# Optimization experiments

Measured on AMD Instinct MI355X. Metric: run time of the kernel, lower is better.

## Reference

```python
import jax, jax.numpy as jnp
import numpy as np

# Dimensions (TinyLlama-like)
B, T = 4, 1024
D = 2048          # hidden_size
H, DH = 32, 64    # heads, head_dim
HK = 8            # kv heads (GQA, n_rep = 4)
RQ, RKV = 32, 32  # per-head SVD ranks
RO, RF = 1024, 1024
I = 5632          # intermediate_size
THETA = 10000.0
EPS = 1e-5


def setup_inputs() -> dict:
    key = jax.random.key(0)
    ks = jax.random.split(key, 16)
    p = lambda k, s: jax.random.normal(k, s, jnp.float32) * 0.02
    return {
        "x": jax.random.normal(ks[0], (B, T, D), jnp.float32),
        "ln1_w": jnp.ones((D,), jnp.float32),
        "ln2_w": jnp.ones((D,), jnp.float32),
        "q_Us": p(ks[1], (H, DH, RQ)),  "q_V": p(ks[2], (H, RQ, D)),
        "k_Us": p(ks[3], (HK, DH, RKV)), "k_V": p(ks[4], (HK, RKV, D)),
        "v_Us": p(ks[5], (HK, DH, RKV)), "v_V": p(ks[6], (HK, RKV, D)),
        "o_Us": p(ks[7], (D, RO)),  "o_V": p(ks[8], (RO, H * DH)),
        "g_Us": p(ks[9], (I, RF)),  "g_V": p(ks[10], (RF, D)),
        "u_Us": p(ks[11], (I, RF)), "u_V": p(ks[12], (RF, D)),
        "d_Us": p(ks[13], (D, RF)), "d_V": p(ks[14], (RF, I)),
    }


def _rms(x, w):
    return x * jax.lax.rsqrt(jnp.mean(x * x, axis=-1, keepdims=True) + EPS) * w


def _rope_cos_sin(t_len, dh, dtype):
    half = dh // 2
    inv_freq = 1.0 / (THETA ** (jnp.arange(half, dtype=jnp.float32) / half))
    ang = jnp.arange(t_len, dtype=jnp.float32)[:, None] * inv_freq[None, :]  # [T, half]
    return jnp.cos(ang).astype(dtype), jnp.sin(ang).astype(dtype)


def _apply_rope(x, cos, sin):
    # x: [B,h,T,Dh], LLaMA half-split rotation
    half = x.shape[-1] // 2
    x1, x2 = x[..., :half], x[..., half:]
    c = cos[None, None]  # [1,1,T,half]
    s = sin[None, None]
    return jnp.concatenate([x1 * c - x2 * s, x2 * c + x1 * s], axis=-1)


def reference(x, ln1_w, ln2_w, q_Us, q_V, k_Us, k_V, v_Us, v_V,
              o_Us, o_V, g_Us, g_V, u_Us, u_V, d_Us, d_V):
    b, t, d = x.shape
    h1 = _rms(x, ln1_w)

    # per-head low-rank projections: y_h = x @ V_h^T @ Us_h^T
    q = jnp.einsum('bhtr,hdr->bhtd', jnp.einsum('btD,hrD->bhtr', h1, q_V), q_Us)  # [B,H,T,Dh]
    k = jnp.einsum('bhtr,hdr->bhtd', jnp.einsum('btD,hrD->bhtr', h1, k_V), k_Us)  # [B,Hk,T,Dh]
    v = jnp.einsum('bhtr,hdr->bhtd', jnp.einsum('btD,hrD->bhtr', h1, v_V), v_Us)

    cos, sin = _rope_cos_sin(t, DH, x.dtype)
    q = _apply_rope(q, cos, sin)
    k = _apply_rope(k, cos, sin)

    n_rep = H // HK
    k = jnp.repeat(k, n_rep, axis=1)  # _repeat_kv
    v = jnp.repeat(v, n_rep, axis=1)

    scale = 1.0 / np.sqrt(DH)
    scores = jnp.einsum('bhtd,bhsd->bhts', q, k) * scale
    causal = jnp.tril(jnp.ones((t, t), bool))
    scores = jnp.where(causal[None, None], scores, jnp.finfo(scores.dtype).min)
    attn = jax.nn.softmax(scores, axis=-1)
    ctx = jnp.einsum('bhts,bhsd->bhtd', attn, v)
    ctx = ctx.transpose(0, 2, 1, 3).reshape(b, t, H * DH)

    # low-rank output proj: o = ctx @ o_V^T @ o_Us^T
    attn_out = jnp.einsum('btr,Dr->btD', jnp.einsum('btk,rk->btr', ctx, o_V), o_Us)
    x = x + attn_out

    # SwiGLU MLP with low-rank factors
    h2 = _rms(x, ln2_w)
    g = jnp.einsum('btr,ir->bti', jnp.einsum('btD,rD->btr', h2, g_V), g_Us)
    u = jnp.einsum('btr,ir->bti', jnp.einsum('btD,rD->btr', h2, u_V), u_Us)
    ff = jax.nn.silu(g) * u
    down = jnp.einsum('btr,Dr->btD', jnp.einsum('bti,ri->btr', ff, d_V), d_Us)
    return x + down
```

## Files before the change

kernel.cpp:

```cpp
#include <hip/hip_runtime.h>
#include <math.h>

typedef unsigned short u16;
typedef unsigned int u32;
typedef __bf16 bf16x8 __attribute__((ext_vector_type(8)));
typedef float f32x4 __attribute__((ext_vector_type(4)));

__device__ __forceinline__ float bf2f(u16 u) {
  union { u32 i; float f; } x; x.i = ((u32)u) << 16; return x.f;
}
__device__ __forceinline__ u16 f2bf(float f) {
  union { float f; u32 i; } x; x.f = f;
  return (u16)((x.i + 0x7fffu + ((x.i >> 16) & 1u)) >> 16);
}

#define GLDS16(gp, lp)                                                        \
  __builtin_amdgcn_global_load_lds(                                           \
      (const __attribute__((address_space(1))) u32*)(gp),                     \
      (__attribute__((address_space(3))) u32*)(lp), 16, 0, 0)

__global__ void detect_k(const u16* __restrict__ w, int* __restrict__ flag) {
  if (threadIdx.x == 0 && blockIdx.x == 0)
    *flag = (w[0] == 0x0000u && w[1] == 0x3F80u) ? 1 : 0;
}

struct CvtArgs {
  const void* src[17];
  u32 dstOff[17];
  u32 blkOff[18];
};

__global__ __launch_bounds__(256) void cvt_all(CvtArgs a, u16* __restrict__ dstB,
                                               const int* __restrict__ flag) {
  int seg = 0;
  const int bx = blockIdx.x;
#pragma unroll 1
  while (bx >= (int)a.blkOff[seg + 1]) seg++;
  const long local = ((long)(bx - a.blkOff[seg]) * 256 + threadIdx.x) * 8;
  u16* dst = dstB + a.dstOff[seg] + local;
  if (*flag) {
    const float* s = (const float*)a.src[seg] + local;
    float4 va = *(const float4*)(s);
    float4 vb = *(const float4*)(s + 4);
    uint4 o; u16* op = (u16*)&o;
    op[0] = f2bf(va.x); op[1] = f2bf(va.y); op[2] = f2bf(va.z); op[3] = f2bf(va.w);
    op[4] = f2bf(vb.x); op[5] = f2bf(vb.y); op[6] = f2bf(vb.z); op[7] = f2bf(vb.w);
    *(uint4*)dst = o;
  } else {
    *(uint4*)dst = *(const uint4*)((const u16*)a.src[seg] + local);
  }
}

__global__ __launch_bounds__(256) void rms_k(const u16* __restrict__ x,
                                             const u16* __restrict__ w,
                                             u16* __restrict__ out) {
  const long row = blockIdx.x;
  const u16* xr = x + row * 2048;
  u16* orow = out + row * 2048;
  const int tid = threadIdx.x;
  const int base = tid * 8;
  uint4 u = *(const uint4*)(xr + base);
  const u16* us = (const u16*)&u;
  float v[8];
  float ss = 0.f;
#pragma unroll
  for (int i = 0; i < 8; i++) { v[i] = bf2f(us[i]); ss += v[i] * v[i]; }
#pragma unroll
  for (int off = 32; off > 0; off >>= 1) ss += __shfl_xor(ss, off);
  __shared__ float red[4];
  if ((tid & 63) == 0) red[tid >> 6] = ss;
  __syncthreads();
  float total = red[0] + red[1] + red[2] + red[3];
  float inv = rsqrtf(total * (1.0f / 2048.0f) + 1e-5f);
  uint4 wv = *(const uint4*)(w + base);
  const u16* wp = (const u16*)&wv;
  uint4 o;
  u16* op = (u16*)&o;
#pragma unroll
  for (int i = 0; i < 8; i++) op[i] = f2bf(v[i] * inv * bf2f(wp[i]));
  *(uint4*)(orow + base) = o;
}

template <int EPI>
__global__ __launch_bounds__(256, 2) void gemm_bt(const u16* __restrict__ A,
                                                  const u16* __restrict__ B,
                                                  void* Cv,
                                                  const u16* R,
                                                  const int* flagp,
                                                  int N, int Klen, int lda, int ldb) {
  __shared__ u16 As[128 * 32];
  __shared__ u16 Bs[128 * 32];
  const int m0 = blockIdx.y * 128;
  const int n0 = blockIdx.x * 128;
  const int tid = threadIdx.x;
  const int wave = tid >> 6;
  const int lane = tid & 63;
  const int wr = (wave >> 1) * 64;
  const int wc = (wave & 1) * 64;
  const int l16 = lane & 15;
  const int quad = lane >> 4;
  u16* C = (u16*)Cv;
  float* Cf = (float*)Cv;
  bool f32o = false;
  if (EPI == 3) f32o = (*flagp != 0);

  f32x4 acc[4][4];
#pragma unroll
  for (int i = 0; i < 4; i++)
#pragma unroll
    for (int j = 0; j < 4; j++) acc[i][j] = (f32x4){0.f, 0.f, 0.f, 0.f};

  const int srow = wave * 16 + (lane >> 2);
  const int scol = (lane & 3) * 8;
  const u16* Ag = A + (long)(m0 + srow) * lda + scol;
  const u16* Bg = B + (long)(n0 + srow) * ldb + scol;
  const long astep = (long)64 * lda;
  const long bstep = (long)64 * ldb;
  u16* Asw = &As[wave * 16 * 32];
  u16* Bsw = &Bs[wave * 16 * 32];

  for (int k0 = 0; k0 < Klen; k0 += 32) {
    GLDS16(Ag + k0, Asw);
    GLDS16(Ag + astep + k0, Asw + 64 * 32);
    GLDS16(Bg + k0, Bsw);
    GLDS16(Bg + bstep + k0, Bsw + 64 * 32);
    __syncthreads();
    bf16x8 af[4], bfr[4];
#pragma unroll
    for (int t = 0; t < 4; t++) {
      af[t]  = *(const bf16x8*)(&As[(wr + t * 16 + l16) * 32 + quad * 8]);
      bfr[t] = *(const bf16x8*)(&Bs[(wc + t * 16 + l16) * 32 + quad * 8]);
    }
#pragma unroll
    for (int i = 0; i < 4; i++)
#pragma unroll
      for (int j = 0; j < 4; j++)
        acc[i][j] = __builtin_amdgcn_mfma_f32_16x16x32_bf16(bfr[j], af[i], acc[i][j], 0, 0, 0);
    __syncthreads();
  }

#pragma unroll
  for (int i = 0; i < 4; i++) {
    const int m = m0 + wr + i * 16 + l16;
#pragma unroll
    for (int j = 0; j < 4; j++) {
      const int n = n0 + wc + j * 16 + quad * 4;
      const long idx = (long)m * N + n;
      float v[4];
#pragma unroll
      for (int r = 0; r < 4; r++) v[r] = acc[i][j][r];
      if (EPI == 1 || EPI == 3) {
        uint2 rr = *(const uint2*)(R + idx);
        const u16* rp = (const u16*)&rr;
#pragma unroll
        for (int r = 0; r < 4; r++) v[r] += bf2f(rp[r]);
      }
      if (EPI == 3 && f32o) {
        float4 o = {v[0], v[1], v[2], v[3]};
        *(float4*)(Cf + idx) = o;
      } else {
        uint2 o; u16* op = (u16*)&o;
#pragma unroll
        for (int r = 0; r < 4; r++) op[r] = f2bf(v[r]);
        *(uint2*)(C + idx) = o;
      }
    }
  }
}

#define STAGE_SILU(buf, k0)                                                   \
  do {                                                                        \
    GLDS16(Ag_ + (k0), &Asg[buf][woff]);                                      \
    GLDS16(Ag_ + astep + (k0), &Asg[buf][woff + 64 * 32]);                    \
    GLDS16(Au_ + (k0), &Asu[buf][woff]);                                      \
    GLDS16(Au_ + astep + (k0), &Asu[buf][woff + 64 * 32]);                    \
    GLDS16(Bg_ + (k0), &Bsg[buf][woff]);                                      \
    GLDS16(Bg_ + bstep + (k0), &Bsg[buf][woff + 64 * 32]);                    \
    GLDS16(Bu_ + (k0), &Bsu[buf][woff]);                                      \
    GLDS16(Bu_ + bstep + (k0), &Bsu[buf][woff + 64 * 32]);                    \
  } while (0)

__global__ __launch_bounds__(256, 2) void gemm_silu(const u16* __restrict__ Agp,
                                                    const u16* __restrict__ Aup,
                                                    const u16* __restrict__ Bgp,
                                                    const u16* __restrict__ Bup,
                                                    u16* __restrict__ C,
                                                    int N, int Klen, int lda, int ldb) {
  __shared__ u16 Asg[2][128 * 32];
  __shared__ u16 Asu[2][128 * 32];
  __shared__ u16 Bsg[2][128 * 32];
  __shared__ u16 Bsu[2][128 * 32];
  const int m0 = blockIdx.y * 128;
  const int n0 = blockIdx.x * 128;
  const int tid = threadIdx.x;
  const int wave = tid >> 6;
  const int lane = tid & 63;
  const int wr = (wave >> 1) * 64;
  const int wc = (wave & 1) * 64;
  const int l16 = lane & 15;
  const int quad = lane >> 4;

  f32x4 ag[4][4], au[4][4];
#pragma unroll
  for (int i = 0; i < 4; i++)
#pragma unroll
    for (int j = 0; j < 4; j++) {
      ag[i][j] = (f32x4){0.f, 0.f, 0.f, 0.f};
      au[i][j] = (f32x4){0.f, 0.f, 0.f, 0.f};
    }

  const int srow = wave * 16 + (lane >> 2);
  const int scol = ((lane & 3) ^ ((lane >> 3) & 3)) * 8;
  const u16* Ag_ = Agp + (long)(m0 + srow) * lda + scol;
  const u16* Au_ = Aup + (long)(m0 + srow) * lda + scol;
  const u16* Bg_ = Bgp + (long)(n0 + srow) * ldb + scol;
  const u16* Bu_ = Bup + (long)(n0 + srow) * ldb + scol;
  const long astep = (long)64 * lda;
  const long bstep = (long)64 * ldb;
  const int woff = wave * 16 * 32;
  const int rsw = (quad ^ ((l16 >> 1) & 3)) * 8;

  const int nk = Klen >> 5;
  STAGE_SILU(0, 0);
  int cur = 0;
  for (int kt = 0; kt < nk; ++kt) {
    if (kt + 1 < nk) {
      STAGE_SILU(cur ^ 1, (kt + 1) << 5);
      asm volatile("s_waitcnt vmcnt(8)" ::: "memory");
    } else {
      asm volatile("s_waitcnt vmcnt(0)" ::: "memory");
    }
    asm volatile("s_barrier" ::: "memory");
    bf16x8 afg[4], afu[4], bfg[4], bfu[4];
#pragma unroll
    for (int t = 0; t < 4; t++) {
      afg[t] = *(const bf16x8*)(&Asg[cur][(wr + t * 16 + l16) * 32 + rsw]);
      afu[t] = *(const bf16x8*)(&Asu[cur][(wr + t * 16 + l16) * 32 + rsw]);
      bfg[t] = *(const bf16x8*)(&Bsg[cur][(wc + t * 16 + l16) * 32 + rsw]);
      bfu[t] = *(const bf16x8*)(&Bsu[cur][(wc + t * 16 + l16) * 32 + rsw]);
    }
#pragma unroll
    for (int i = 0; i < 4; i++)
#pragma unroll
      for (int j = 0; j < 4; j++) {
        ag[i][j] = __builtin_amdgcn_mfma_f32_16x16x32_bf16(bfg[j], afg[i], ag[i][j], 0, 0, 0);
        au[i][j] = __builtin_amdgcn_mfma_f32_16x16x32_bf16(bfu[j], afu[i], au[i][j], 0, 0, 0);
      }
    asm volatile("s_barrier" ::: "memory");
    cur ^= 1;
  }

#pragma unroll
  for (int i = 0; i < 4; i++) {
    const int m = m0 + wr + i * 16 + l16;
#pragma unroll
    for (int j = 0; j < 4; j++) {
      const int n = n0 + wc + j * 16 + quad * 4;
      const long idx = (long)m * N + n;
      uint2 o; u16* op = (u16*)&o;
#pragma unroll
      for (int r = 0; r < 4; r++) {
        float g = ag[i][j][r];
        float v = au[i][j][r] * g / (1.f + __expf(-g));
        op[r] = f2bf(v);
      }
      *(uint2*)(C + idx) = o;
    }
  }
}

__global__ __launch_bounds__(256) void combine2(const u16* __restrict__ a,
                                                const u16* __restrict__ b,
                                                u16* __restrict__ o) {
  const long i = ((long)blockIdx.x * 256 + threadIdx.x) * 8;
  uint4 ua = *(const uint4*)(a + i);
  uint4 ub = *(const uint4*)(b + i);
  const u16* pa = (const u16*)&ua;
  const u16* pb = (const u16*)&ub;
  uint4 uo; u16* po = (u16*)&uo;
#pragma unroll
  for (int j = 0; j < 8; j++) po[j] = f2bf(bf2f(pa[j]) + bf2f(pb[j]));
  *(uint4*)(o + i) = uo;
}

__global__ __launch_bounds__(256) void expand_k(const u16* __restrict__ rbuf,
                                                int rstride,
                                                const u16* __restrict__ Us,
                                                u16* __restrict__ out,
                                                int nheads, int doRope) {
  const int tok = blockIdx.x;
  const int wave = threadIdx.x >> 6;
  const int d = threadIdx.x & 63;
  const int h = blockIdx.y * 4 + wave;
  const int b = tok >> 10;
  const int t = tok & 1023;
  const u16* up = Us + ((long)h * 64 + d) * 32;
  const u16* rp = rbuf + (long)tok * rstride + h * 32;
  float s = 0.f;
#pragma unroll
  for (int c = 0; c < 4; c++) {
    uint4 uu = *(const uint4*)(up + c * 8);
    uint4 rr = *(const uint4*)(rp + c * 8);
    const u16* u8p = (const u16*)&uu;
    const u16* r8p = (const u16*)&rr;
#pragma unroll
    for (int i = 0; i < 8; i++) s += bf2f(u8p[i]) * bf2f(r8p[i]);
  }
  if (doRope) {
    const int j = d & 31;
    float inv = powf(10000.0f, -(float)j * (1.0f / 32.0f));
    float ang = (float)t * inv;
    float sn, cs;
    sincosf(ang, &sn, &cs);
    float partner = __shfl_xor(s, 32);
    s = (d < 32) ? (s * cs - partner * sn) : (s * cs + partner * sn);
  }
  out[(((long)(b * nheads + h)) * 1024 + t) * 64 + d] = f2bf(s);
}

__global__ __launch_bounds__(256) void vT_k(const u16* __restrict__ vbuf,
                                            u16* __restrict__ vT) {
  __shared__ u16 tile[64][72];
  const int b = blockIdx.z, kh = blockIdx.y;
  const int t0 = blockIdx.x * 64;
  const int tid = threadIdx.x;
  const int r = tid >> 2;
  const int c = (tid & 3) * 16;
  const u16* src = vbuf + ((long)(b * 8 + kh) * 1024 + t0 + r) * 64 + c;
  *(uint4*)&tile[r][c] = *(const uint4*)src;
  *(uint4*)&tile[r][c + 8] = *(const uint4*)(src + 8);
  __syncthreads();
  u16 tmp[16];
#pragma unroll
  for (int i = 0; i < 16; i++) tmp[i] = tile[c + i][r];
  u16* dst = vT + ((long)(b * 8 + kh) * 64 + r) * 1024 + t0 + c;
  *(uint4*)dst = *(uint4*)&tmp[0];
  *(uint4*)(dst + 8) = *(uint4*)&tmp[8];
}

#define ATS 72

__global__ __launch_bounds__(256, 2) void attn_mfma(const u16* __restrict__ q,
                                                    const u16* __restrict__ k,
                                                    const u16* __restrict__ vT,
                                                    u16* __restrict__ ctx) {
  __shared__ u16 Ks[64 * ATS];
  __shared__ u16 Vts[64 * ATS];
  __shared__ u16 Plds[4][16 * ATS];
  const int bx = blockIdx.x;
  const int h = blockIdx.y;
  const int b = blockIdx.z;
  const int kh = h >> 2;
  const int qlo = bx * 64;
  const int qhi = (15 - bx) * 64;
  const int tid = threadIdx.x;
  const int wave = tid >> 6;
  const int lane = tid & 63;
  const int l16 = lane & 15;
  const int quad = lane >> 4;

  const u16* qb = q + ((long)(b * 32 + h) * 1024) * 64;
  const u16* kb = k + ((long)(b * 8 + kh) * 1024) * 64;
  const u16* vb = vT + ((long)(b * 8 + kh) * 64) * 1024;

  bf16x8 qfl[2], qfh[2];
  {
    const u16* qp = qb + (long)(qlo + wave * 16 + l16) * 64 + quad * 8;
    qfl[0] = *(const bf16x8*)(qp);
    qfl[1] = *(const bf16x8*)(qp + 32);
    qp = qb + (long)(qhi + wave * 16 + l16) * 64 + quad * 8;
    qfh[0] = *(const bf16x8*)(qp);
    qfh[1] = *(const bf16x8*)(qp + 32);
  }

  float ml[4], ll[4], mh[4], lh[4];
  f32x4 ol[4], oh[4];
#pragma unroll
  for (int r = 0; r < 4; r++) { ml[r] = -1e30f; ll[r] = 0.f; mh[r] = -1e30f; lh[r] = 0.f; }
#pragma unroll
  for (int j = 0; j < 4; j++) { ol[j] = (f32x4){0.f, 0.f, 0.f, 0.f}; oh[j] = ol[j]; }

  const int srow = tid >> 2;
  const int sc0 = (tid & 3) * 16;
  int s0 = 0;

  auto process = [&](const bf16x8* qf, float* m, float* l, f32x4* oacc, int qtb) {
    f32x4 s[4];
#pragma unroll
    for (int t = 0; t < 4; t++) {
      s[t] = (f32x4){0.f, 0.f, 0.f, 0.f};
      const u16* kr = &Ks[(t * 16 + l16) * ATS + quad * 8];
      bf16x8 b0 = *(const bf16x8*)(kr);
      bf16x8 b1 = *(const bf16x8*)(kr + 32);
      s[t] = __builtin_amdgcn_mfma_f32_16x16x32_bf16(qf[0], b0, s[t], 0, 0, 0);
      s[t] = __builtin_amdgcn_mfma_f32_16x16x32_bf16(qf[1], b1, s[t], 0, 0, 0);
    }
#pragma unroll
    for (int t = 0; t < 4; t++) s[t] *= 0.125f;
    if (s0 == qtb) {
#pragma unroll
      for (int t = 0; t < 4; t++)
#pragma unroll
        for (int r = 0; r < 4; r++)
          if (s0 + t * 16 + l16 > qtb + wave * 16 + quad * 4 + r) s[t][r] = -1e30f;
    }
    float p[4][4];
#pragma unroll
    for (int r = 0; r < 4; r++) {
      float mx = fmaxf(fmaxf(s[0][r], s[1][r]), fmaxf(s[2][r], s[3][r]));
#pragma unroll
      for (int off = 1; off < 16; off <<= 1) mx = fmaxf(mx, __shfl_xor(mx, off));
      const float mnew = fmaxf(m[r], mx);
      const float alpha = __expf(m[r] - mnew);
      float ps = 0.f;
#pragma unroll
      for (int t = 0; t < 4; t++) { p[t][r] = __expf(s[t][r] - mnew); ps += p[t][r]; }
#pragma unroll
      for (int off = 1; off < 16; off <<= 1) ps += __shfl_xor(ps, off);
      l[r] = l[r] * alpha + ps;
      m[r] = mnew;
#pragma unroll
      for (int j = 0; j < 4; j++) oacc[j][r] *= alpha;
    }
    u16* pw = &Plds[wave][0];
#pragma unroll
    for (int t = 0; t < 4; t++)
#pragma unroll
      for (int r = 0; r < 4; r++)
        pw[(quad * 4 + r) * ATS + t * 16 + l16] = f2bf(p[t][r]);
    bf16x8 pf0 = *(const bf16x8*)(&pw[l16 * ATS + quad * 8]);
    bf16x8 pf1 = *(const bf16x8*)(&pw[l16 * ATS + 32 + quad * 8]);
#pragma unroll
    for (int j = 0; j < 4; j++) {
      const u16* vr = &Vts[(j * 16 + l16) * ATS + quad * 8];
      bf16x8 v0 = *(const bf16x8*)(vr);
      bf16x8 v1 = *(const bf16x8*)(vr + 32);
      oacc[j] = __builtin_amdgcn_mfma_f32_16x16x32_bf16(pf0, v0, oacc[j], 0, 0, 0);
      oacc[j] = __builtin_amdgcn_mfma_f32_16x16x32_bf16(pf1, v1, oacc[j], 0, 0, 0);
    }
  };

  for (s0 = 0; s0 <= qhi; s0 += 64) {
    __syncthreads();
    {
      const u16* kp = kb + (long)(s0 + srow) * 64 + sc0;
      *(uint4*)&Ks[srow * ATS + sc0] = *(const uint4*)kp;
      *(uint4*)&Ks[srow * ATS + sc0 + 8] = *(const uint4*)(kp + 8);
      const u16* vp = vb + (long)srow * 1024 + s0 + sc0;
      *(uint4*)&Vts[srow * ATS + sc0] = *(const uint4*)vp;
      *(uint4*)&Vts[srow * ATS + sc0 + 8] = *(const uint4*)(vp + 8);
    }
    __syncthreads();
    process(qfh, mh, lh, oh, qhi);
    if (s0 <= qlo) process(qfl, ml, ll, ol, qlo);
  }

#pragma unroll
  for (int r = 0; r < 4; r++) {
    const int rowl = qlo + wave * 16 + quad * 4 + r;
    const int rowh = qhi + wave * 16 + quad * 4 + r;
    const float il = 1.f / ll[r];
    const float ih = 1.f / lh[r];
#pragma unroll
    for (int j = 0; j < 4; j++) {
      ctx[(((long)(b * 1024 + rowl)) * 32 + h) * 64 + j * 16 + l16] = f2bf(ol[j][r] * il);
      ctx[(((long)(b * 1024 + rowh)) * 32 + h) * 64 + j * 16 + l16] = f2bf(oh[j][r] * ih);
    }
  }
}

extern "C" void kernel_launch(void* const* d_in, const int* in_sizes, int n_in,
                              void* d_out, int out_size, void* d_ws, size_t ws_size,
                              hipStream_t stream) {
  char* ws = (char*)d_ws;
  u16* cb = (u16*)ws;
  u16* cx    = cb + 0;
  u16* cln1  = cb + 8388608;
  u16* cln2  = cb + 8390656;
  u16* cqUs  = cb + 8392704;
  u16* ckUs  = cb + 8458240;
  u16* cvUs  = cb + 8474624;
  u16* cqkvV = cb + 8491008;
  u16* coUs  = cb + 11636736;
  u16* coV   = cb + 13733888;
  u16* cguV  = cb + 15831040;
  u16* cgUs  = cb + 20025344;
  u16* cuUs  = cb + 25792512;
  u16* cdUs  = cb + 31559680;
  u16* cdV   = cb + 33656832;

  char* P = ws + 78848000;
  u16* h1    = (u16*)(P + 0);
  u16* qkvr  = (u16*)(P + 16777216);
  u16* qp0   = (u16*)(P + 33554432);
  u16* qp1   = (u16*)(P + 46137344);
  u16* qbuf  = (u16*)(P + 33554432);
  u16* kbuf  = (u16*)(P + 50331648);
  u16* vbuf  = (u16*)(P + 54525952);
  u16* ctx   = (u16*)(P + 58720256);
  u16* vbufT = (u16*)(P + 75497472);
  u16* orr   = (u16*)(P + 75497472);
  u16* xmid  = (u16*)(P + 83886080);
  u16* op0   = (u16*)(P + 0);
  u16* op1   = (u16*)(P + 8388608);
  u16* h2    = (u16*)(P + 0);
  u16* gur   = (u16*)(P + 16777216);
  u16* gbuf  = (u16*)(P + 33554432);
  u16* dp0   = (u16*)(P + 0);
  u16* dp1   = (u16*)(P + 8388608);
  u16* dr    = (u16*)(P + 16777216);
  int* flag  = (int*)(ws + 179511296);

  const dim3 blk(256);
  detect_k<<<1, 64, 0, stream>>>((const u16*)d_in[1], flag);

  CvtArgs ca;
  const u32 dOff[17] = {0u, 8388608u, 8390656u, 8392704u, 8491008u, 8458240u,
                        10588160u, 8474624u, 11112448u, 11636736u, 13733888u,
                        20025344u, 15831040u, 25792512u, 17928192u, 31559680u,
                        33656832u};
  const u32 nblk[17] = {4096u, 1u, 1u, 32u, 1024u, 8u, 256u, 8u, 256u, 1024u,
                        1024u, 2816u, 1024u, 2816u, 1024u, 1024u, 2816u};
  u32 cum = 0;
  for (int i = 0; i < 17; i++) {
    ca.src[i] = d_in[i];
    ca.dstOff[i] = dOff[i];
    ca.blkOff[i] = cum;
    cum += nblk[i];
  }
  ca.blkOff[17] = cum;
  cvt_all<<<cum, blk, 0, stream>>>(ca, cb, flag);

  rms_k<<<4096, blk, 0, stream>>>(cx, cln1, h1);
  gemm_bt<0><<<dim3(12, 32), blk, 0, stream>>>(h1, cqkvV, qp0, nullptr, nullptr, 1536, 1024, 2048, 2048);
  gemm_bt<0><<<dim3(12, 32), blk, 0, stream>>>(h1 + 1024, cqkvV + 1024, qp1, nullptr, nullptr, 1536, 1024, 2048, 2048);
  combine2<<<3072, blk, 0, stream>>>(qp0, qp1, qkvr);
  expand_k<<<dim3(4096, 8), blk, 0, stream>>>(qkvr, 1536, cqUs, qbuf, 32, 1);
  expand_k<<<dim3(4096, 2), blk, 0, stream>>>(qkvr + 1024, 1536, ckUs, kbuf, 8, 1);
  expand_k<<<dim3(4096, 2), blk, 0, stream>>>(qkvr + 1280, 1536, cvUs, vbuf, 8, 0);
  vT_k<<<dim3(16, 8, 4), blk, 0, stream>>>(vbuf, vbufT);
  attn_mfma<<<dim3(8, 32, 4), blk, 0, stream>>>(qbuf, kbuf, vbufT, ctx);
  gemm_bt<0><<<dim3(8, 32), blk, 0, stream>>>(ctx, coV, op0, nullptr, nullptr, 1024, 1024, 2048, 2048);
  gemm_bt<0><<<dim3(8, 32), blk, 0, stream>>>(ctx + 1024, coV + 1024, op1, nullptr, nullptr, 1024, 1024, 2048, 2048);
  combine2<<<2048, blk, 0, stream>>>(op0, op1, orr);
  gemm_bt<1><<<dim3(16, 32), blk, 0, stream>>>(orr, coUs, xmid, cx, nullptr, 2048, 1024, 1024, 1024);
  rms_k<<<4096, blk, 0, stream>>>(xmid, cln2, h2);
  gemm_bt<0><<<dim3(16, 32), blk, 0, stream>>>(h2, cguV, gur, nullptr, nullptr, 2048, 2048, 2048, 2048);
  gemm_silu<<<dim3(44, 32), blk, 0, stream>>>(gur, gur + 1024, cgUs, cuUs, gbuf, 5632, 1024, 2048, 1024);
  gemm_bt<0><<<dim3(8, 32), blk, 0, stream>>>(gbuf, cdV, dp0, nullptr, nullptr, 1024, 2816, 5632, 5632);
  gemm_bt<0><<<dim3(8, 32), blk, 0, stream>>>(gbuf + 2816, cdV + 2816, dp1, nullptr, nullptr, 1024, 2816, 5632, 5632);
  combine2<<<2048, blk, 0, stream>>>(dp0, dp1, dr);
  gemm_bt<3><<<dim3(16, 32), blk, 0, stream>>>(dr, cdUs, d_out, xmid, flag, 2048, 1024, 1024, 1024);
}
```

Measured before the change: 854.5 us.

## Split gate and up GEMM across separate waves in fused SiLU kernel

The fused gate/up SiLU GEMM now uses 512 threads. Waves 0-3 compute the gate product and waves 4-7 compute the up product, each holding half the accumulators. The up results are passed to the gate waves through shared memory before the SiLU epilogue. This halves per-wave register pressure and doubles the waves per tile, aiming for better latency hiding. The cost is an extra shared-memory exchange and a block-wide sync at the end.

Result: no change. 851.8 us (-0.3%).

```diff
diff --git a/kernel.cpp b/kernel.cpp
--- a/kernel.cpp
+++ b/kernel.cpp
@@ -170,44 +170,38 @@
 
 #define STAGE_SILU(buf, k0)                                                   \
   do {                                                                        \
-    GLDS16(Ag_ + (k0), &Asg[buf][woff]);                                      \
-    GLDS16(Ag_ + astep + (k0), &Asg[buf][woff + 64 * 32]);                    \
-    GLDS16(Au_ + (k0), &Asu[buf][woff]);                                      \
-    GLDS16(Au_ + astep + (k0), &Asu[buf][woff + 64 * 32]);                    \
-    GLDS16(Bg_ + (k0), &Bsg[buf][woff]);                                      \
-    GLDS16(Bg_ + bstep + (k0), &Bsg[buf][woff + 64 * 32]);                    \
-    GLDS16(Bu_ + (k0), &Bsu[buf][woff]);                                      \
-    GLDS16(Bu_ + bstep + (k0), &Bsu[buf][woff + 64 * 32]);                    \
+    GLDS16(Ag_ + (k0), &SH[buf][0][woff]);                                    \
+    GLDS16(Au_ + (k0), &SH[buf][1][woff]);                                    \
+    GLDS16(Bg_ + (k0), &SH[buf][2][woff]);                                    \
+    GLDS16(Bu_ + (k0), &SH[buf][3][woff]);                                    \
   } while (0)
 
-__global__ __launch_bounds__(256, 2) void gemm_silu(const u16* __restrict__ Agp,
+__global__ __launch_bounds__(512, 4) void gemm_silu(const u16* __restrict__ Agp,
                                                     const u16* __restrict__ Aup,
                                                     const u16* __restrict__ Bgp,
                                                     const u16* __restrict__ Bup,
                                                     u16* __restrict__ C,
                                                     int N, int Klen, int lda, int ldb) {
-  __shared__ u16 Asg[2][128 * 32];
-  __shared__ u16 Asu[2][128 * 32];
-  __shared__ u16 Bsg[2][128 * 32];
-  __shared__ u16 Bsu[2][128 * 32];
+  __shared__ u16 SH[2][4][128 * 32];
   const int m0 = blockIdx.y * 128;
   const int n0 = blockIdx.x * 128;
   const int tid = threadIdx.x;
   const int wave = tid >> 6;
   const int lane = tid & 63;
-  const int wr = (wave >> 1) * 64;
-  const int wc = (wave & 1) * 64;
+  const int wid = wave & 3;
+  const int isU = wave >> 2;
+  const int wr = (wid >> 1) * 64;
+  const int wc = (wid & 1) * 64;
   const int l16 = lane & 15;
   const int quad = lane >> 4;
-
-  f32x4 ag[4][4], au[4][4];
+  const int matA = isU;
+  const int matB = 2 + isU;
+
+  f32x4 acc[4][4];
 #pragma unroll
   for (int i = 0; i < 4; i++)
 #pragma unroll
-    for (int j = 0; j < 4; j++) {
-      ag[i][j] = (f32x4){0.f, 0.f, 0.f, 0.f};
-      au[i][j] = (f32x4){0.f, 0.f, 0.f, 0.f};
-    }
+    for (int j = 0; j < 4; j++) acc[i][j] = (f32x4){0.f, 0.f, 0.f, 0.f};
 
   const int srow = wave * 16 + (lane >> 2);
   const int scol = ((lane & 3) ^ ((lane >> 3) & 3)) * 8;
@@ -215,9 +209,7 @@
   const u16* Au_ = Aup + (long)(m0 + srow) * lda + scol;
   const u16* Bg_ = Bgp + (long)(n0 + srow) * ldb + scol;
   const u16* Bu_ = Bup + (long)(n0 + srow) * ldb + scol;
-  const long astep = (long)64 * lda;
-  const long bstep = (long)64 * ldb;
-  const int woff = wave * 16 * 32;
+  const int woff = wave * 512;
   const int rsw = (quad ^ ((l16 >> 1) & 3)) * 8;
 
   const int nk = Klen >> 5;
@@ -226,45 +218,55 @@
   for (int kt = 0; kt < nk; ++kt) {
     if (kt + 1 < nk) {
       STAGE_SILU(cur ^ 1, (kt + 1) << 5);
-      asm volatile("s_waitcnt vmcnt(8)" ::: "memory");
+      asm volatile("s_waitcnt vmcnt(4)" ::: "memory");
     } else {
       asm volatile("s_waitcnt vmcnt(0)" ::: "memory");
     }
     asm volatile("s_barrier" ::: "memory");
-    bf16x8 afg[4], afu[4], bfg[4], bfu[4];
+    bf16x8 af[4], bfr[4];
 #pragma unroll
     for (int t = 0; t < 4; t++) {
-      afg[t] = *(const bf16x8*)(&Asg[cur][(wr + t * 16 + l16) * 32 + rsw]);
-      afu[t] = *(const bf16x8*)(&Asu[cur][(wr + t * 16 + l16) * 32 + rsw]);
-      bfg[t] = *(const bf16x8*)(&Bsg[cur][(wc + t * 16 + l16) * 32 + rsw]);
-      bfu[t] = *(const bf16x8*)(&Bsu[cur][(wc + t * 16 + l16) * 32 + rsw]);
+      af[t]  = *(const bf16x8*)(&SH[cur][matA][(wr + t * 16 + l16) * 32 + rsw]);
+      bfr[t] = *(const bf16x8*)(&SH[cur][matB][(wc + t * 16 + l16) * 32 + rsw]);
     }
 #pragma unroll
     for (int i = 0; i < 4; i++)
 #pragma unroll
-      for (int j = 0; j < 4; j++) {
-        ag[i][j] = __builtin_amdgcn_mfma_f32_16x16x32_bf16(bfg[j], afg[i], ag[i][j], 0, 0, 0);
-        au[i][j] = __builtin_amdgcn_mfma_f32_16x16x32_bf16(bfu[j], afu[i], au[i][j], 0, 0, 0);
-      }
+      for (int j = 0; j < 4; j++)
+        acc[i][j] = __builtin_amdgcn_mfma_f32_16x16x32_bf16(bfr[j], af[i], acc[i][j], 0, 0, 0);
     asm volatile("s_barrier" ::: "memory");
     cur ^= 1;
   }
 
-#pragma unroll
-  for (int i = 0; i < 4; i++) {
-    const int m = m0 + wr + i * 16 + l16;
-#pragma unroll
-    for (int j = 0; j < 4; j++) {
-      const int n = n0 + wc + j * 16 + quad * 4;
-      const long idx = (long)m * N + n;
-      uint2 o; u16* op = (u16*)&o;
-#pragma unroll
-      for (int r = 0; r < 4; r++) {
-        float g = ag[i][j][r];
-        float v = au[i][j][r] * g / (1.f + __expf(-g));
-        op[r] = f2bf(v);
+  float* xch = (float*)&SH[0][0][0];
+  if (isU) {
+    float* w = xch + wid * 4096 + lane * 4;
+#pragma unroll
+    for (int i = 0; i < 4; i++)
+#pragma unroll
+      for (int j = 0; j < 4; j++)
+        *(f32x4*)(w + (i * 4 + j) * 256) = acc[i][j];
+  }
+  __syncthreads();
+  if (!isU) {
+    const float* w = xch + wid * 4096 + lane * 4;
+#pragma unroll
+    for (int i = 0; i < 4; i++) {
+      const int m = m0 + wr + i * 16 + l16;
+#pragma unroll
+      for (int j = 0; j < 4; j++) {
+        const int n = n0 + wc + j * 16 + quad * 4;
+        const long idx = (long)m * N + n;
+        f32x4 uv = *(const f32x4*)(w + (i * 4 + j) * 256);
+        uint2 o; u16* op = (u16*)&o;
+#pragma unroll
+        for (int r = 0; r < 4; r++) {
+          float g = acc[i][j][r];
+          float v = uv[r] * g / (1.f + __expf(-g));
+          op[r] = f2bf(v);
+        }
+        *(uint2*)(C + idx) = o;
       }
-      *(uint2*)(C + idx) = o;
     }
   }
 }
@@ -546,7 +548,7 @@
   gemm_bt<1><<<dim3(16, 32), blk, 0, stream>>>(orr, coUs, xmid, cx, nullptr, 2048, 1024, 1024, 1024);
   rms_k<<<4096, blk, 0, stream>>>(xmid, cln2, h2);
   gemm_bt<0><<<dim3(16, 32), blk, 0, stream>>>(h2, cguV, gur, nullptr, nullptr, 2048, 2048, 2048, 2048);
-  gemm_silu<<<dim3(44, 32), blk, 0, stream>>>(gur, gur + 1024, cgUs, cuUs, gbuf, 5632, 1024, 2048, 1024);
+  gemm_silu<<<dim3(44, 32), dim3(512), 0, stream>>>(gur, gur + 1024, cgUs, cuUs, gbuf, 5632, 1024, 2048, 1024);
   gemm_bt<0><<<dim3(8, 32), blk, 0, stream>>>(gbuf, cdV, dp0, nullptr, nullptr, 1024, 2816, 5632, 5632);
   gemm_bt<0><<<dim3(8, 32), blk, 0, stream>>>(gbuf + 2816, cdV + 2816, dp1, nullptr, nullptr, 1024, 2816, 5632, 5632);
   combine2<<<2048, blk, 0, stream>>>(dp0, dp1, dr);
```
